# Kernel tuning notes

Measured on AMD Instinct MI355X. Metric: run time of the kernel, lower is better.

Reference implementation:

```python
import jax, jax.numpy as jnp
import numpy as np

D_MODEL = 1024
NUM_HEADS = 16
SEQ_LEN = 2048
WINDOW_SIZES = (5, 10, 20, 40)


def _avg_gaussian_mask(seq_len, dtype=jnp.float32):
    # mask[i,j] = exp(-(i-j)^2/(2 w^2)) if j <= i else 0; averaged over 4 windows.
    i = jnp.arange(seq_len, dtype=dtype)[:, None]
    j = jnp.arange(seq_len, dtype=dtype)[None, :]
    d2 = (i - j) ** 2
    lower = (j <= i)
    masks = [jnp.where(lower, jnp.exp(-d2 / (2.0 * w * w)), 0.0) for w in WINDOW_SIZES]
    return sum(masks) / len(WINDOW_SIZES)  # [S, S]


def setup_inputs() -> dict:
    key = jax.random.key(0)
    ks = jax.random.split(key, 11)
    B, S, D = 2, SEQ_LEN, D_MODEL
    std = 1.0 / np.sqrt(D)
    inp = {
        "Q": jax.random.normal(ks[0], (B, S, D), jnp.float32),
        "K": jax.random.normal(ks[1], (B, S, D), jnp.float32),
        "V": jax.random.normal(ks[2], (B, S, D), jnp.float32),
        "Wq": jax.random.uniform(ks[3], (D, D), jnp.float32, -std, std),
        "bq": jax.random.uniform(ks[4], (D,), jnp.float32, -std, std),
        "Wk": jax.random.uniform(ks[5], (D, D), jnp.float32, -std, std),
        "bk": jax.random.uniform(ks[6], (D,), jnp.float32, -std, std),
        "Wv": jax.random.uniform(ks[7], (D, D), jnp.float32, -std, std),
        "bv": jax.random.uniform(ks[8], (D,), jnp.float32, -std, std),
        "Wo": jax.random.uniform(ks[9], (D, D), jnp.float32, -std, std),
        "bo": jax.random.uniform(ks[10], (D,), jnp.float32, -std, std),
    }
    return inp


def reference(Q, K, V, Wq, bq, Wk, bk, Wv, bv, Wo, bo):
    B, S, D = Q.shape
    H, dk = NUM_HEADS, D // NUM_HEADS

    def proj(x, W, b):
        # torch Linear: x @ W^T + b, then split heads -> [B, H, S, dk]
        y = x @ W.T + b
        return y.reshape(B, S, H, dk).transpose(0, 2, 1, 3)

    q = proj(Q, Wq, bq)
    k = proj(K, Wk, bk)
    v = proj(V, Wv, bv)

    # mean over mask dim of (scores + mask_m) == scores + mean(mask)
    avg_mask = _avg_gaussian_mask(S, q.dtype)  # [S, S]
    scores = jnp.einsum('bhqd,bhkd->bhqk', q, k) / jnp.sqrt(jnp.asarray(dk, q.dtype))
    scores = scores + avg_mask  # broadcast over [B, H]
    probs = jax.nn.softmax(scores, axis=-1)
    out = jnp.einsum('bhqk,bhkd->bhqd', probs, v)
    out = out.transpose(0, 2, 1, 3).reshape(B, S, D)
    return out @ Wo.T + bo
```

## Files before the change

### kernel.cpp

```cpp
#include <hip/hip_runtime.h>
#include <hip/hip_bf16.h>


#define S_LEN 2048
#define D_MODEL 1024
#define NHEADS 16
#define DK 64
#define BATCH 2
#define M_ROWS (BATCH * S_LEN)
#define LOG2E 1.4426950408889634f

typedef float f32x4 __attribute__((ext_vector_type(4)));
typedef short s16x8 __attribute__((ext_vector_type(8)));
typedef unsigned short u16x4 __attribute__((ext_vector_type(4)));
typedef unsigned u32x4 __attribute__((ext_vector_type(4)));

__device__ __forceinline__ unsigned short f2bf(float f) {
    unsigned u = __builtin_bit_cast(unsigned, f);
    u = (u + 0x7FFFu + ((u >> 16) & 1u)) >> 16;
    return (unsigned short)u;
}

__device__ __forceinline__ float fast_exp2(float x) {
    float r;
    asm("v_exp_f32 %0, %1" : "=v"(r) : "v"(x));
    return r;
}

__device__ __forceinline__ unsigned cvt_pk_bf16(float a, float b) {
    unsigned r;
    asm("v_cvt_pk_bf16_f32 %0, %1, %2" : "=v"(r) : "v"(a), "v"(b));
    return r;
}

#define GLD16(gptr, lptr)                                                     \
    __builtin_amdgcn_global_load_lds(                                         \
        (const __attribute__((address_space(1))) void*)(gptr),                \
        (__attribute__((address_space(3))) void*)(lptr), 16, 0, 0)

__global__ __launch_bounds__(256) void convert_kernel(
    const float* __restrict__ Q, const float* __restrict__ K,
    const float* __restrict__ V,
    const float* __restrict__ Wq, const float* __restrict__ Wk,
    const float* __restrict__ Wv, const float* __restrict__ Wo,
    unsigned short* __restrict__ Qb, unsigned short* __restrict__ Kb,
    unsigned short* __restrict__ Vb,
    unsigned short* __restrict__ Wqb, unsigned short* __restrict__ Wkb,
    unsigned short* __restrict__ Wvb, unsigned short* __restrict__ Wob,
    float* __restrict__ mtab)
{
    const int XN = M_ROWS * D_MODEL / 8;
    const int WN = D_MODEL * D_MODEL / 8;
    const int TOT = 3 * XN + 4 * WN;
    int i = blockIdx.x * 256 + threadIdx.x;
    if (i >= TOT) {
        int d = i - TOT;
        if (d < S_LEN) {
            float d2 = (float)d * (float)d;
            mtab[d] = LOG2E * 0.25f * (__expf(-d2 * (1.0f / 50.0f)) +
                                       __expf(-d2 * (1.0f / 200.0f)) +
                                       __expf(-d2 * (1.0f / 800.0f)) +
                                       __expf(-d2 * (1.0f / 3200.0f)));
        }
        return;
    }
    const float* src;
    unsigned short* dst;
    int off;
    if (i < 3 * XN) {
        if (i < XN)          { src = Q; dst = Qb; off = i; }
        else if (i < 2 * XN) { src = K; dst = Kb; off = i - XN; }
        else                 { src = V; dst = Vb; off = i - 2 * XN; }
    } else {
        int j = i - 3 * XN;
        if (j < WN)          { src = Wq; dst = Wqb; off = j; }
        else if (j < 2 * WN) { src = Wk; dst = Wkb; off = j - WN; }
        else if (j < 3 * WN) { src = Wv; dst = Wvb; off = j - 2 * WN; }
        else                 { src = Wo; dst = Wob; off = j - 3 * WN; }
    }
    f32x4 v0 = *(const f32x4*)(src + (size_t)off * 8);
    f32x4 v1 = *(const f32x4*)(src + (size_t)off * 8 + 4);
    s16x8 o;
#pragma unroll
    for (int j = 0; j < 4; ++j) {
        o[j]     = (short)f2bf(v0[j]);
        o[j + 4] = (short)f2bf(v1[j]);
    }
    *(s16x8*)(dst + (size_t)off * 8) = o;
}

__device__ __forceinline__ void gemm_core_128(
    const unsigned short* __restrict__ A, const unsigned short* __restrict__ B,
    unsigned short* As, unsigned short* Bs,
    int m0, int n0, int K, int tid, f32x4 acc[4][4])
{
    const int wid  = tid >> 6;
    const int lane = tid & 63;
    const int g    = lane >> 4;
    const int c    = lane & 15;
    const int wm   = wid >> 1;
    const int wn   = wid & 1;

    const int srow   = tid >> 3;
    const int schunk = tid & 7;

    for (int kt = 0; kt < K / 64; ++kt) {
        const int k0 = kt * 64;
        __syncthreads();
#pragma unroll
        for (int r = 0; r < 4; ++r) {
            const int row = r * 32 + srow;
            GLD16(A + (size_t)(m0 + row) * K + k0 + schunk * 8,
                  &As[(r * 256 + wid * 64) * 8]);
        }
#pragma unroll
        for (int r = 0; r < 4; ++r) {
            const int row = r * 32 + srow;
            GLD16(B + (size_t)(n0 + row) * K + k0 + schunk * 8,
                  &Bs[(r * 256 + wid * 64) * 8]);
        }
        __syncthreads();

        s16x8 a[2][4];
#pragma unroll
        for (int ks = 0; ks < 2; ++ks)
#pragma unroll
            for (int mf = 0; mf < 4; ++mf)
                a[ks][mf] = *(const s16x8*)
                    &As[(wm * 64 + mf * 16 + c) * 64 + ks * 32 + g * 8];
#pragma unroll
        for (int ks = 0; ks < 2; ++ks) {
#pragma unroll
            for (int nf = 0; nf < 4; ++nf) {
                s16x8 b = *(const s16x8*)
                    &Bs[(wn * 64 + nf * 16 + c) * 64 + ks * 32 + g * 8];
#pragma unroll
                for (int mf = 0; mf < 4; ++mf)
                    acc[mf][nf] = __builtin_amdgcn_mfma_f32_16x16x32_bf16(
                        a[ks][mf], b, acc[mf][nf], 0, 0, 0);
            }
        }
    }
}

__global__ __launch_bounds__(256) void proj_gemm(
    const unsigned short* __restrict__ Qx, const unsigned short* __restrict__ Kx,
    const unsigned short* __restrict__ Vx,
    const unsigned short* __restrict__ Wq, const unsigned short* __restrict__ Wk,
    const unsigned short* __restrict__ Wv,
    const float* __restrict__ bq, const float* __restrict__ bk,
    const float* __restrict__ bv,
    unsigned short* __restrict__ qo, unsigned short* __restrict__ ko,
    unsigned short* __restrict__ vo)
{
    const int z = blockIdx.z;
    const unsigned short* X = (z == 0) ? Qx : (z == 1) ? Kx : Vx;
    const unsigned short* W = (z == 0) ? Wq : (z == 1) ? Wk : Wv;
    const float* bias       = (z == 0) ? bq : (z == 1) ? bk : bv;
    unsigned short* out     = (z == 0) ? qo : (z == 1) ? ko : vo;
    const float scale = (z == 0) ? (0.125f * LOG2E) : 1.0f;

    __shared__ unsigned short As[128 * 64];
    __shared__ unsigned short Bs[128 * 64];

    const int tid = threadIdx.x;
    const int flat = blockIdx.y * 32 + blockIdx.x;
    const int sw   = (flat & 7) * 32 + (flat >> 3);
    const int m0   = (sw & 31) * 128;
    const int n0   = (sw >> 5) * 128;

    f32x4 acc[4][4];
#pragma unroll
    for (int i = 0; i < 4; ++i)
#pragma unroll
        for (int j = 0; j < 4; ++j) acc[i][j] = (f32x4){0.f, 0.f, 0.f, 0.f};

    gemm_core_128(X, W, As, Bs, m0, n0, D_MODEL, tid, acc);

    const int lane = tid & 63;
    const int g    = lane >> 4;
    const int c    = lane & 15;
    const int wm   = (tid >> 6) >> 1;
    const int wn   = (tid >> 6) & 1;

#pragma unroll
    for (int mf = 0; mf < 4; ++mf) {
#pragma unroll
        for (int nf = 0; nf < 4; ++nf) {
            const int o = n0 + wn * 64 + nf * 16 + c;
            const float bv_ = bias[o];
            const int h  = o >> 6;
            const int dd = o & 63;
#pragma unroll
            for (int r = 0; r < 4; ++r) {
                const int m = m0 + wm * 64 + mf * 16 + g * 4 + r;
                const int b = m >> 11;
                const int s = m & (S_LEN - 1);
                const float val = (acc[mf][nf][r] + bv_) * scale;
                out[(((size_t)(b * NHEADS + h)) * S_LEN + s) * DK + dd] = f2bf(val);
            }
        }
    }
}

__global__ __launch_bounds__(256) void out_gemm(
    const unsigned short* __restrict__ A,
    const unsigned short* __restrict__ W,
    const float* __restrict__ bias,
    float* __restrict__ out)
{
    __shared__ unsigned short As[128 * 64];
    __shared__ unsigned short Bs[128 * 64];

    const int tid = threadIdx.x;
    const int flat = blockIdx.y * 32 + blockIdx.x;
    const int sw   = (flat & 7) * 32 + (flat >> 3);
    const int m0   = (sw & 31) * 128;
    const int n0   = (sw >> 5) * 128;

    f32x4 acc[4][4];
#pragma unroll
    for (int i = 0; i < 4; ++i)
#pragma unroll
        for (int j = 0; j < 4; ++j) acc[i][j] = (f32x4){0.f, 0.f, 0.f, 0.f};

    gemm_core_128(A, W, As, Bs, m0, n0, D_MODEL, tid, acc);

    const int lane = tid & 63;
    const int g    = lane >> 4;
    const int c    = lane & 15;
    const int wm   = (tid >> 6) >> 1;
    const int wn   = (tid >> 6) & 1;

#pragma unroll
    for (int mf = 0; mf < 4; ++mf) {
#pragma unroll
        for (int nf = 0; nf < 4; ++nf) {
            const int o = n0 + wn * 64 + nf * 16 + c;
            const float bv_ = bias[o];
#pragma unroll
            for (int r = 0; r < 4; ++r) {
                const int m = m0 + wm * 64 + mf * 16 + g * 4 + r;
                out[(size_t)m * D_MODEL + o] = acc[mf][nf][r] + bv_;
            }
        }
    }
}

#define SWZ(row) ((((row) & 7) ^ ((((row) >> 3) & 1) << 2)) << 4)

__global__ __launch_bounds__(512) void attn_kernel(
    const unsigned short* __restrict__ qh,
    const unsigned short* __restrict__ kh,
    const unsigned short* __restrict__ vh,
    const float* __restrict__ mask_tab,
    unsigned short* __restrict__ attn_out)
{
    __shared__ float mtab[S_LEN];
    __shared__ unsigned short Kt[2][64 * 64];
    __shared__ unsigned short Vt[2][64 * 64];

    const int tid  = threadIdx.x;
    const int wid  = tid >> 6;
    const int lane = tid & 63;
    const int g    = lane >> 4;
    const int c    = lane & 15;

    const int flat = blockIdx.y * 16 + blockIdx.x;
    const int sw   = (flat & 7) * 64 + (flat >> 3);
    const int bh   = sw >> 4;
    const int bx   = sw & 15;
    const int b    = bh >> 4;
    const int h    = bh & 15;
    const int q0w  = bx * 128 + wid * 16;

    *(f32x4*)&mtab[tid * 4] = *(const f32x4*)&mask_tab[tid * 4];

    const size_t head_off = (size_t)bh * S_LEN * DK;
    const unsigned short* qp = qh + head_off;
    const unsigned short* kp = kh + head_off;
    const unsigned short* vp = vh + head_off;

    s16x8 aq[2];
    {
        const unsigned short* qrow = qp + (size_t)(q0w + c) * DK;
        aq[0] = *(const s16x8*)(qrow + g * 8);
        aq[1] = *(const s16x8*)(qrow + 32 + g * 8);
    }

    f32x4 acc_o[4];
#pragma unroll
    for (int nf = 0; nf < 4; ++nf) acc_o[nf] = (f32x4){0.f, 0.f, 0.f, 0.f};
    f32x4 lsum = (f32x4){0.f, 0.f, 0.f, 0.f};

    int krow_nf[4];
#pragma unroll
    for (int nf = 0; nf < 4; ++nf)
        krow_nf[nf] = ((c >> 2) << 3) + ((nf & 1) << 2) + (c & 3) + ((nf >> 1) << 5);

    const int srowK = tid >> 3;
    const int soffE = (tid & 7) * 8;
    const int vd0   = (tid & 31) * 2;
    const int vkq   = (tid >> 5) * 4;

    s16x8 kreg;
    unsigned vreg[4];

    kreg = *(const s16x8*)&kp[(size_t)srowK * DK + soffE];
#pragma unroll
    for (int i = 0; i < 4; ++i)
        vreg[i] = *(const unsigned*)&vp[(size_t)(vkq + i) * DK + vd0];
    {
        *(s16x8*)((char*)Kt[0] + srowK * 128 + ((soffE * 2) ^ SWZ(srowK))) = kreg;
        u16x4 lo4, hi4;
#pragma unroll
        for (int i = 0; i < 4; ++i) {
            lo4[i] = (unsigned short)vreg[i];
            hi4[i] = (unsigned short)(vreg[i] >> 16);
        }
        *(u16x4*)((char*)Vt[0] + vd0 * 128 + ((vkq * 2) ^ SWZ(vd0)))           = lo4;
        *(u16x4*)((char*)Vt[0] + (vd0 + 1) * 128 + ((vkq * 2) ^ SWZ(vd0 + 1))) = hi4;
    }
    kreg = *(const s16x8*)&kp[(size_t)(64 + srowK) * DK + soffE];
#pragma unroll
    for (int i = 0; i < 4; ++i)
        vreg[i] = *(const unsigned*)&vp[(size_t)(64 + vkq + i) * DK + vd0];
    __syncthreads();

    const int NT = S_LEN / 64;
    for (int kt = 0; kt < NT; ++kt) {
        const int k0 = kt * 64;
        const int cur = kt & 1;
        const unsigned short* Kc = Kt[cur];
        const unsigned short* Vc = Vt[cur];

        if (kt + 1 < NT) {
            unsigned short* Kn = Kt[cur ^ 1];
            unsigned short* Vn = Vt[cur ^ 1];
            *(s16x8*)((char*)Kn + srowK * 128 + ((soffE * 2) ^ SWZ(srowK))) = kreg;
            u16x4 lo4, hi4;
#pragma unroll
            for (int i = 0; i < 4; ++i) {
                lo4[i] = (unsigned short)vreg[i];
                hi4[i] = (unsigned short)(vreg[i] >> 16);
            }
            *(u16x4*)((char*)Vn + vd0 * 128 + ((vkq * 2) ^ SWZ(vd0)))           = lo4;
            *(u16x4*)((char*)Vn + (vd0 + 1) * 128 + ((vkq * 2) ^ SWZ(vd0 + 1))) = hi4;
            if (kt + 2 < NT) {
                const int k2 = k0 + 128;
                kreg = *(const s16x8*)&kp[(size_t)(k2 + srowK) * DK + soffE];
#pragma unroll
                for (int i = 0; i < 4; ++i)
                    vreg[i] = *(const unsigned*)&vp[(size_t)(k2 + vkq + i) * DK + vd0];
            }
        }

        f32x4 st[4];
        __builtin_amdgcn_s_setprio(1);
#pragma unroll
        for (int nf = 0; nf < 4; ++nf) {
            st[nf] = (f32x4){0.f, 0.f, 0.f, 0.f};
            const int row = krow_nf[nf];
#pragma unroll
            for (int f = 0; f < 2; ++f) {
                s16x8 kf = *(const s16x8*)((const char*)Kc + row * 128 +
                                           ((f * 64 + g * 16) ^ SWZ(row)));
                st[nf] = __builtin_amdgcn_mfma_f32_16x16x32_bf16(
                    kf, aq[f], st[nf], 0, 0, 0);
            }
        }
        __builtin_amdgcn_s_setprio(0);

        const int diff = q0w - k0;
        if (diff >= -15 && diff <= 510) {
            const int dbase = q0w + c - k0 - g * 8;
#pragma unroll
            for (int nf = 0; nf < 4; ++nf) {
                const int koff = ((nf & 1) << 2) + ((nf >> 1) << 5);
#pragma unroll
                for (int r = 0; r < 4; ++r) {
                    const int d = dbase - koff - r;
                    if (d >= 0) st[nf][r] += mtab[d];
                }
            }
        }

#pragma unroll
        for (int nf = 0; nf < 4; ++nf)
#pragma unroll
            for (int r = 0; r < 4; ++r)
                st[nf][r] = fast_exp2(st[nf][r]);
        lsum += (st[0] + st[1]) + (st[2] + st[3]);

        __builtin_amdgcn_s_setprio(1);
#pragma unroll
        for (int f = 0; f < 2; ++f) {
            u32x4 w;
            w[0] = cvt_pk_bf16(st[2 * f][0],     st[2 * f][1]);
            w[1] = cvt_pk_bf16(st[2 * f][2],     st[2 * f][3]);
            w[2] = cvt_pk_bf16(st[2 * f + 1][0], st[2 * f + 1][1]);
            w[3] = cvt_pk_bf16(st[2 * f + 1][2], st[2 * f + 1][3]);
            s16x8 pa = __builtin_bit_cast(s16x8, w);
#pragma unroll
            for (int nf = 0; nf < 4; ++nf) {
                const int row = nf * 16 + c;
                s16x8 vb = *(const s16x8*)((const char*)Vc + row * 128 +
                                           ((f * 64 + g * 16) ^ SWZ(row)));
                acc_o[nf] = __builtin_amdgcn_mfma_f32_16x16x32_bf16(
                    pa, vb, acc_o[nf], 0, 0, 0);
            }
        }
        __builtin_amdgcn_s_setprio(0);

        __syncthreads();
    }

    float l = (lsum[0] + lsum[1]) + (lsum[2] + lsum[3]);
    l += __shfl_xor(l, 16);
    l += __shfl_xor(l, 32);
    f32x4 linv;
#pragma unroll
    for (int r = 0; r < 4; ++r) linv[r] = 1.0f / __shfl(l, g * 4 + r);
#pragma unroll
    for (int nf = 0; nf < 4; ++nf) {
#pragma unroll
        for (int r = 0; r < 4; ++r) {
            const int i_glob = q0w + g * 4 + r;
            const int d = nf * 16 + c;
            attn_out[((size_t)(b * S_LEN + i_glob)) * D_MODEL + h * DK + d] =
                f2bf(acc_o[nf][r] * linv[r]);
        }
    }
}

extern "C" void kernel_launch(void* const* d_in, const int* in_sizes, int n_in,
                              void* d_out, int out_size, void* d_ws, size_t ws_size,
                              hipStream_t stream) {
    const float* Q  = (const float*)d_in[0];
    const float* K  = (const float*)d_in[1];
    const float* V  = (const float*)d_in[2];
    const float* Wq = (const float*)d_in[3];
    const float* bq = (const float*)d_in[4];
    const float* Wk = (const float*)d_in[5];
    const float* bk = (const float*)d_in[6];
    const float* Wv = (const float*)d_in[7];
    const float* bv = (const float*)d_in[8];
    const float* Wo = (const float*)d_in[9];
    const float* bo = (const float*)d_in[10];
    float* out = (float*)d_out;

    const size_t XE = (size_t)M_ROWS * D_MODEL;
    const size_t WE = (size_t)D_MODEL * D_MODEL;
    unsigned short* qh  = (unsigned short*)d_ws;
    unsigned short* kh  = qh + XE;
    unsigned short* vh  = kh + XE;
    unsigned short* ah  = vh + XE;
    unsigned short* Qb  = ah + XE;
    unsigned short* Kb  = Qb + XE;
    unsigned short* Vb  = Kb + XE;
    unsigned short* Wqb = Vb + XE;
    unsigned short* Wkb = Wqb + WE;
    unsigned short* Wvb = Wkb + WE;
    unsigned short* Wob = Wvb + WE;
    float* mtab = (float*)(Wob + WE);

    convert_kernel<<<dim3((3 * XE / 8 + 4 * WE / 8) / 256 + 8), 256, 0, stream>>>(
        Q, K, V, Wq, Wk, Wv, Wo, Qb, Kb, Vb, Wqb, Wkb, Wvb, Wob, mtab);
    proj_gemm<<<dim3(32, 8, 3), 256, 0, stream>>>(
        Qb, Kb, Vb, Wqb, Wkb, Wvb, bq, bk, bv, qh, kh, vh);
    attn_kernel<<<dim3(16, 32), 512, 0, stream>>>(
        qh, kh, vh, mtab, ah);
    out_gemm<<<dim3(32, 8), 256, 0, stream>>>(
        ah, Wob, bo, out);
}
```

Measured before the change: 130.4 us.

## Process two query fragments per wave in attention to reuse K/V LDS reads

The attention block now uses 4 waves of 256 threads instead of 8 waves, and each wave handles 32 query rows (two 16-row fragments) instead of 16. Every K and V fragment read from LDS now feeds two MFMAs, halving LDS read traffic per unit of compute. Staging is reorganised so each thread loads twice as much K/V per tile, and V uses a new swizzle suited to 8-element writes. The cost is more registers per thread and fewer waves per block, which leaves less latency hiding and fewer waves to overlap exp work with MFMA.

```diff
diff --git a/kernel.cpp b/kernel.cpp
--- a/kernel.cpp
+++ b/kernel.cpp
@@ -12,7 +12,7 @@
 
 typedef float f32x4 __attribute__((ext_vector_type(4)));
 typedef short s16x8 __attribute__((ext_vector_type(8)));
-typedef unsigned short u16x4 __attribute__((ext_vector_type(4)));
+typedef unsigned short u16x8 __attribute__((ext_vector_type(8)));
 typedef unsigned u32x4 __attribute__((ext_vector_type(4)));
 
 __device__ __forceinline__ unsigned short f2bf(float f) {
@@ -247,9 +247,10 @@
     }
 }
 
-#define SWZ(row) ((((row) & 7) ^ ((((row) >> 3) & 1) << 2)) << 4)
-
-__global__ __launch_bounds__(512) void attn_kernel(
+#define SWZ(row)  ((((row) & 7) ^ ((((row) >> 3) & 1) << 2)) << 4)
+#define VSWZ(row) ((((row) >> 1) & 7) << 4)
+
+__global__ __launch_bounds__(256) void attn_kernel(
     const unsigned short* __restrict__ qh,
     const unsigned short* __restrict__ kh,
     const unsigned short* __restrict__ vh,
@@ -272,59 +273,69 @@
     const int bx   = sw & 15;
     const int b    = bh >> 4;
     const int h    = bh & 15;
-    const int q0w  = bx * 128 + wid * 16;
-
-    *(f32x4*)&mtab[tid * 4] = *(const f32x4*)&mask_tab[tid * 4];
+    const int q0w  = bx * 128 + wid * 32;
+
+    *(f32x4*)&mtab[tid * 8]     = *(const f32x4*)&mask_tab[tid * 8];
+    *(f32x4*)&mtab[tid * 8 + 4] = *(const f32x4*)&mask_tab[tid * 8 + 4];
 
     const size_t head_off = (size_t)bh * S_LEN * DK;
     const unsigned short* qp = qh + head_off;
     const unsigned short* kp = kh + head_off;
     const unsigned short* vp = vh + head_off;
 
-    s16x8 aq[2];
-    {
-        const unsigned short* qrow = qp + (size_t)(q0w + c) * DK;
-        aq[0] = *(const s16x8*)(qrow + g * 8);
-        aq[1] = *(const s16x8*)(qrow + 32 + g * 8);
-    }
-
-    f32x4 acc_o[4];
-#pragma unroll
-    for (int nf = 0; nf < 4; ++nf) acc_o[nf] = (f32x4){0.f, 0.f, 0.f, 0.f};
-    f32x4 lsum = (f32x4){0.f, 0.f, 0.f, 0.f};
+    s16x8 aq[2][2];
+#pragma unroll
+    for (int qf = 0; qf < 2; ++qf) {
+        const unsigned short* qrow = qp + (size_t)(q0w + qf * 16 + c) * DK;
+        aq[qf][0] = *(const s16x8*)(qrow + g * 8);
+        aq[qf][1] = *(const s16x8*)(qrow + 32 + g * 8);
+    }
+
+    f32x4 acc_o[2][4];
+#pragma unroll
+    for (int qf = 0; qf < 2; ++qf)
+#pragma unroll
+        for (int nf = 0; nf < 4; ++nf) acc_o[qf][nf] = (f32x4){0.f, 0.f, 0.f, 0.f};
+    f32x4 lsum[2];
+    lsum[0] = (f32x4){0.f, 0.f, 0.f, 0.f};
+    lsum[1] = (f32x4){0.f, 0.f, 0.f, 0.f};
 
     int krow_nf[4];
 #pragma unroll
     for (int nf = 0; nf < 4; ++nf)
         krow_nf[nf] = ((c >> 2) << 3) + ((nf & 1) << 2) + (c & 3) + ((nf >> 1) << 5);
 
-    const int srowK = tid >> 3;
-    const int soffE = (tid & 7) * 8;
-    const int vd0   = (tid & 31) * 2;
-    const int vkq   = (tid >> 5) * 4;
-
-    s16x8 kreg;
-    unsigned vreg[4];
-
-    kreg = *(const s16x8*)&kp[(size_t)srowK * DK + soffE];
-#pragma unroll
-    for (int i = 0; i < 4; ++i)
-        vreg[i] = *(const unsigned*)&vp[(size_t)(vkq + i) * DK + vd0];
+    const int srowK  = tid >> 2;
+    const int kchunk = (tid & 3) * 16;
+    const int vd0    = (tid & 31) * 2;
+    const int vk8    = (tid >> 5) * 8;
+
+    s16x8 kr0, kr1;
+    unsigned vr[8];
+
+    kr0 = *(const s16x8*)&kp[(size_t)srowK * DK + kchunk];
+    kr1 = *(const s16x8*)&kp[(size_t)srowK * DK + kchunk + 8];
+#pragma unroll
+    for (int i = 0; i < 8; ++i)
+        vr[i] = *(const unsigned*)&vp[(size_t)(vk8 + i) * DK + vd0];
     {
-        *(s16x8*)((char*)Kt[0] + srowK * 128 + ((soffE * 2) ^ SWZ(srowK))) = kreg;
-        u16x4 lo4, hi4;
-#pragma unroll
-        for (int i = 0; i < 4; ++i) {
-            lo4[i] = (unsigned short)vreg[i];
-            hi4[i] = (unsigned short)(vreg[i] >> 16);
-        }
-        *(u16x4*)((char*)Vt[0] + vd0 * 128 + ((vkq * 2) ^ SWZ(vd0)))           = lo4;
-        *(u16x4*)((char*)Vt[0] + (vd0 + 1) * 128 + ((vkq * 2) ^ SWZ(vd0 + 1))) = hi4;
-    }
-    kreg = *(const s16x8*)&kp[(size_t)(64 + srowK) * DK + soffE];
-#pragma unroll
-    for (int i = 0; i < 4; ++i)
-        vreg[i] = *(const unsigned*)&vp[(size_t)(64 + vkq + i) * DK + vd0];
+        char* kb = (char*)Kt[0] + srowK * 128;
+        *(s16x8*)(kb + ((kchunk * 2) ^ SWZ(srowK)))      = kr0;
+        *(s16x8*)(kb + ((kchunk * 2 + 16) ^ SWZ(srowK))) = kr1;
+        u16x8 lo, hi8;
+#pragma unroll
+        for (int i = 0; i < 8; ++i) {
+            lo[i]  = (unsigned short)vr[i];
+            hi8[i] = (unsigned short)(vr[i] >> 16);
+        }
+        *(u16x8*)((char*)Vt[0] + vd0 * 128 + ((vk8 * 2) ^ VSWZ(vd0)))           = lo;
+        *(u16x8*)((char*)Vt[0] + (vd0 + 1) * 128 + ((vk8 * 2) ^ VSWZ(vd0 + 1))) = hi8;
+    }
+    kr0 = *(const s16x8*)&kp[(size_t)(64 + srowK) * DK + kchunk];
+    kr1 = *(const s16x8*)&kp[(size_t)(64 + srowK) * DK + kchunk + 8];
+#pragma unroll
+    for (int i = 0; i < 8; ++i)
+        vr[i] = *(const unsigned*)&vp[(size_t)(64 + vk8 + i) * DK + vd0];
     __syncthreads();
 
     const int NT = S_LEN / 64;
@@ -335,79 +346,97 @@
         const unsigned short* Vc = Vt[cur];
 
         if (kt + 1 < NT) {
-            unsigned short* Kn = Kt[cur ^ 1];
-            unsigned short* Vn = Vt[cur ^ 1];
-            *(s16x8*)((char*)Kn + srowK * 128 + ((soffE * 2) ^ SWZ(srowK))) = kreg;
-            u16x4 lo4, hi4;
-#pragma unroll
-            for (int i = 0; i < 4; ++i) {
-                lo4[i] = (unsigned short)vreg[i];
-                hi4[i] = (unsigned short)(vreg[i] >> 16);
-            }
-            *(u16x4*)((char*)Vn + vd0 * 128 + ((vkq * 2) ^ SWZ(vd0)))           = lo4;
-            *(u16x4*)((char*)Vn + (vd0 + 1) * 128 + ((vkq * 2) ^ SWZ(vd0 + 1))) = hi4;
+            char* kb = (char*)Kt[cur ^ 1] + srowK * 128;
+            *(s16x8*)(kb + ((kchunk * 2) ^ SWZ(srowK)))      = kr0;
+            *(s16x8*)(kb + ((kchunk * 2 + 16) ^ SWZ(srowK))) = kr1;
+            u16x8 lo, hi8;
+#pragma unroll
+            for (int i = 0; i < 8; ++i) {
+                lo[i]  = (unsigned short)vr[i];
+                hi8[i] = (unsigned short)(vr[i] >> 16);
+            }
+            *(u16x8*)((char*)Vt[cur ^ 1] + vd0 * 128 +
+                      ((vk8 * 2) ^ VSWZ(vd0))) = lo;
+            *(u16x8*)((char*)Vt[cur ^ 1] + (vd0 + 1) * 128 +
+                      ((vk8 * 2) ^ VSWZ(vd0 + 1))) = hi8;
             if (kt + 2 < NT) {
                 const int k2 = k0 + 128;
-                kreg = *(const s16x8*)&kp[(size_t)(k2 + srowK) * DK + soffE];
-#pragma unroll
-                for (int i = 0; i < 4; ++i)
-                    vreg[i] = *(const unsigned*)&vp[(size_t)(k2 + vkq + i) * DK + vd0];
-            }
-        }
-
-        f32x4 st[4];
+                kr0 = *(const s16x8*)&kp[(size_t)(k2 + srowK) * DK + kchunk];
+                kr1 = *(const s16x8*)&kp[(size_t)(k2 + srowK) * DK + kchunk + 8];
+#pragma unroll
+                for (int i = 0; i < 8; ++i)
+                    vr[i] = *(const unsigned*)&vp[(size_t)(k2 + vk8 + i) * DK + vd0];
+            }
+        }
+
+        f32x4 st[2][4];
         __builtin_amdgcn_s_setprio(1);
 #pragma unroll
         for (int nf = 0; nf < 4; ++nf) {
-            st[nf] = (f32x4){0.f, 0.f, 0.f, 0.f};
+            st[0][nf] = (f32x4){0.f, 0.f, 0.f, 0.f};
+            st[1][nf] = (f32x4){0.f, 0.f, 0.f, 0.f};
             const int row = krow_nf[nf];
 #pragma unroll
             for (int f = 0; f < 2; ++f) {
                 s16x8 kf = *(const s16x8*)((const char*)Kc + row * 128 +
                                            ((f * 64 + g * 16) ^ SWZ(row)));
-                st[nf] = __builtin_amdgcn_mfma_f32_16x16x32_bf16(
-                    kf, aq[f], st[nf], 0, 0, 0);
+                st[0][nf] = __builtin_amdgcn_mfma_f32_16x16x32_bf16(
+                    kf, aq[0][f], st[0][nf], 0, 0, 0);
+                st[1][nf] = __builtin_amdgcn_mfma_f32_16x16x32_bf16(
+                    kf, aq[1][f], st[1][nf], 0, 0, 0);
             }
         }
         __builtin_amdgcn_s_setprio(0);
 
         const int diff = q0w - k0;
-        if (diff >= -15 && diff <= 510) {
-            const int dbase = q0w + c - k0 - g * 8;
-#pragma unroll
-            for (int nf = 0; nf < 4; ++nf) {
-                const int koff = ((nf & 1) << 2) + ((nf >> 1) << 5);
-#pragma unroll
-                for (int r = 0; r < 4; ++r) {
-                    const int d = dbase - koff - r;
-                    if (d >= 0) st[nf][r] += mtab[d];
+        if (diff >= -31 && diff <= 510) {
+#pragma unroll
+            for (int qf = 0; qf < 2; ++qf) {
+                const int dbase = q0w + qf * 16 + c - k0 - g * 8;
+#pragma unroll
+                for (int nf = 0; nf < 4; ++nf) {
+                    const int koff = ((nf & 1) << 2) + ((nf >> 1) << 5);
+#pragma unroll
+                    for (int r = 0; r < 4; ++r) {
+                        const int d = dbase - koff - r;
+                        if (d >= 0) st[qf][nf][r] += mtab[d];
+                    }
                 }
             }
         }
 
-#pragma unroll
-        for (int nf = 0; nf < 4; ++nf)
-#pragma unroll
-            for (int r = 0; r < 4; ++r)
-                st[nf][r] = fast_exp2(st[nf][r]);
-        lsum += (st[0] + st[1]) + (st[2] + st[3]);
+        u32x4 pa[2][2];
+#pragma unroll
+        for (int qf = 0; qf < 2; ++qf) {
+#pragma unroll
+            for (int nf = 0; nf < 4; ++nf)
+#pragma unroll
+                for (int r = 0; r < 4; ++r)
+                    st[qf][nf][r] = fast_exp2(st[qf][nf][r]);
+            lsum[qf] += (st[qf][0] + st[qf][1]) + (st[qf][2] + st[qf][3]);
+#pragma unroll
+            for (int f = 0; f < 2; ++f) {
+                pa[qf][f][0] = cvt_pk_bf16(st[qf][2 * f][0],     st[qf][2 * f][1]);
+                pa[qf][f][1] = cvt_pk_bf16(st[qf][2 * f][2],     st[qf][2 * f][3]);
+                pa[qf][f][2] = cvt_pk_bf16(st[qf][2 * f + 1][0], st[qf][2 * f + 1][1]);
+                pa[qf][f][3] = cvt_pk_bf16(st[qf][2 * f + 1][2], st[qf][2 * f + 1][3]);
+            }
+        }
 
         __builtin_amdgcn_s_setprio(1);
 #pragma unroll
         for (int f = 0; f < 2; ++f) {
-            u32x4 w;
-            w[0] = cvt_pk_bf16(st[2 * f][0],     st[2 * f][1]);
-            w[1] = cvt_pk_bf16(st[2 * f][2],     st[2 * f][3]);
-            w[2] = cvt_pk_bf16(st[2 * f + 1][0], st[2 * f + 1][1]);
-            w[3] = cvt_pk_bf16(st[2 * f + 1][2], st[2 * f + 1][3]);
-            s16x8 pa = __builtin_bit_cast(s16x8, w);
+            s16x8 pa0 = __builtin_bit_cast(s16x8, pa[0][f]);
+            s16x8 pa1 = __builtin_bit_cast(s16x8, pa[1][f]);
 #pragma unroll
             for (int nf = 0; nf < 4; ++nf) {
                 const int row = nf * 16 + c;
                 s16x8 vb = *(const s16x8*)((const char*)Vc + row * 128 +
-                                           ((f * 64 + g * 16) ^ SWZ(row)));
-                acc_o[nf] = __builtin_amdgcn_mfma_f32_16x16x32_bf16(
-                    pa, vb, acc_o[nf], 0, 0, 0);
+                                           ((f * 64 + g * 16) ^ VSWZ(row)));
+                acc_o[0][nf] = __builtin_amdgcn_mfma_f32_16x16x32_bf16(
+                    pa0, vb, acc_o[0][nf], 0, 0, 0);
+                acc_o[1][nf] = __builtin_amdgcn_mfma_f32_16x16x32_bf16(
+                    pa1, vb, acc_o[1][nf], 0, 0, 0);
             }
         }
         __builtin_amdgcn_s_setprio(0);
@@ -415,20 +444,23 @@
         __syncthreads();
     }
 
-    float l = (lsum[0] + lsum[1]) + (lsum[2] + lsum[3]);
-    l += __shfl_xor(l, 16);
-    l += __shfl_xor(l, 32);
-    f32x4 linv;
-#pragma unroll
-    for (int r = 0; r < 4; ++r) linv[r] = 1.0f / __shfl(l, g * 4 + r);
-#pragma unroll
-    for (int nf = 0; nf < 4; ++nf) {
-#pragma unroll
-        for (int r = 0; r < 4; ++r) {
-            const int i_glob = q0w + g * 4 + r;
-            const int d = nf * 16 + c;
-            attn_out[((size_t)(b * S_LEN + i_glob)) * D_MODEL + h * DK + d] =
-                f2bf(acc_o[nf][r] * linv[r]);
+#pragma unroll
+    for (int qf = 0; qf < 2; ++qf) {
+        float l = (lsum[qf][0] + lsum[qf][1]) + (lsum[qf][2] + lsum[qf][3]);
+        l += __shfl_xor(l, 16);
+        l += __shfl_xor(l, 32);
+        f32x4 linv;
+#pragma unroll
+        for (int r = 0; r < 4; ++r) linv[r] = 1.0f / __shfl(l, g * 4 + r);
+#pragma unroll
+        for (int nf = 0; nf < 4; ++nf) {
+#pragma unroll
+            for (int r = 0; r < 4; ++r) {
+                const int i_glob = q0w + qf * 16 + g * 4 + r;
+                const int d = nf * 16 + c;
+                attn_out[((size_t)(b * S_LEN + i_glob)) * D_MODEL + h * DK + d] =
+                    f2bf(acc_o[qf][nf][r] * linv[r]);
+            }
         }
     }
 }
@@ -468,7 +500,7 @@
         Q, K, V, Wq, Wk, Wv, Wo, Qb, Kb, Vb, Wqb, Wkb, Wvb, Wob, mtab);
     proj_gemm<<<dim3(32, 8, 3), 256, 0, stream>>>(
         Qb, Kb, Vb, Wqb, Wkb, Wvb, bq, bk, bv, qh, kh, vh);
-    attn_kernel<<<dim3(16, 32), 512, 0, stream>>>(
+    attn_kernel<<<dim3(16, 32), 256, 0, stream>>>(
         qh, kh, vh, mtab, ah);
     out_gemm<<<dim3(32, 8), 256, 0, stream>>>(
         ah, Wob, bo, out);
```

Result: slower. 147.7 us (+13.3%).
